# Kernel optimization log

Measured on AMD Instinct MI355X. Metric: run time of the kernel, lower is better.

## Reference

```python
import jax, jax.numpy as jnp
import numpy as np

N = 20000      # nodes
E = 320000     # edges (before self loops)
IN = 128       # in_channels
HID = 256      # hidden_channels
HEADS = 8
C = HID // HEADS  # 32 per-head dim
L = 4          # num_gat_layers
BN_EPS = 1e-5
LN_EPS = 1e-5


def setup_inputs() -> dict:
    key = jax.random.key(0)
    ks = iter(jax.random.split(key, 64))
    def rn(shape, s=0.05):
        return jax.random.normal(next(ks), shape, jnp.float32) * s
    inp = {
        'x': jax.random.normal(next(ks), (N, IN), jnp.float32),
        'edge_index': jax.random.randint(next(ks), (2, E), 0, N),
        # FeatureMLP
        'mlp_w1': rn((IN, HID)), 'mlp_b1': jnp.zeros((HID,), jnp.float32),
        'bn1_g': jnp.ones((HID,), jnp.float32), 'bn1_b': jnp.zeros((HID,), jnp.float32),
        'mlp_w2': rn((HID, HID)), 'mlp_b2': jnp.zeros((HID,), jnp.float32),
        'bn2_g': jnp.ones((HID,), jnp.float32), 'bn2_b': jnp.zeros((HID,), jnp.float32),
        'mlp_w3': rn((HID, HID)), 'mlp_b3': jnp.zeros((HID,), jnp.float32),
        # stacked GATv2 layer params [L, ...]
        'gat_wl': rn((L, HID, HID)), 'gat_bl': jnp.zeros((L, HID), jnp.float32),
        'gat_wr': rn((L, HID, HID)), 'gat_br': jnp.zeros((L, HID), jnp.float32),
        'gat_att': rn((L, HEADS, C)), 'gat_bias': jnp.zeros((L, HID), jnp.float32),
        'ln_g': jnp.ones((L, HID), jnp.float32), 'ln_b': jnp.zeros((L, HID), jnp.float32),
        'head_w1': rn((2 * HID, HID)), 'head_b1': jnp.zeros((HID,), jnp.float32),
        'hbn1_g': jnp.ones((HID,), jnp.float32), 'hbn1_b': jnp.zeros((HID,), jnp.float32),
        'head_w2': rn((HID, HID // 2)), 'head_b2': jnp.zeros((HID // 2,), jnp.float32),
        'hbn2_g': jnp.ones((HID // 2,), jnp.float32), 'hbn2_b': jnp.zeros((HID // 2,), jnp.float32),
        'head_w3': rn((HID // 2, HID // 4)), 'head_b3': jnp.zeros((HID // 4,), jnp.float32),
        'head_w4': rn((HID // 4, 1)), 'head_b4': jnp.zeros((1,), jnp.float32),
    }
    return inp


def _lrelu01(v):
    return jax.nn.leaky_relu(v, 0.1)


def _bn_eval(v, g, b):
    # eval-mode BatchNorm1d with running_mean=0, running_var=1
    return v * (g / jnp.sqrt(1.0 + BN_EPS)) + b


def _layernorm(v, g, b):
    mu = jnp.mean(v, axis=-1, keepdims=True)
    var = jnp.mean((v - mu) ** 2, axis=-1, keepdims=True)
    return (v - mu) / jnp.sqrt(var + LN_EPS) * g + b


def _gatv2(x, src, dst, Wl, bl, Wr, br, att, bias):
    n = x.shape[0]
    xl = (x @ Wl + bl).reshape(n, HEADS, C)   # source transform
    xr = (x @ Wr + br).reshape(n, HEADS, C)   # target transform
    # per-edge attention logits (GATv2): a . LeakyReLU(x_l[src] + x_r[dst])
    e = jax.nn.leaky_relu(xl[src] + xr[dst], 0.2)          # [E, H, C]
    logits = jnp.einsum('ehc,hc->eh', e, att)               # [E, H]
    # segment softmax over destination nodes
    m = jax.ops.segment_max(logits, dst, num_segments=n)    # [N, H]
    a = jnp.exp(logits - m[dst])
    s = jax.ops.segment_sum(a, dst, num_segments=n)
    alpha = a / (s[dst] + 1e-16)                            # [E, H]
    out = jax.ops.segment_sum(xl[src] * alpha[:, :, None], dst, num_segments=n)
    return out.reshape(n, HID) + bias


def _forward(x, mlp_w1, mlp_b1, bn1_g, bn1_b, mlp_w2, mlp_b2, bn2_g, bn2_b,
             mlp_w3, mlp_b3, gat_wl, gat_bl, gat_wr, gat_br, gat_att, gat_bias,
             ln_g, ln_b, head_w1, head_b1, hbn1_g, hbn1_b, head_w2, head_b2,
             hbn2_g, hbn2_b, head_w3, head_b3, head_w4, head_b4, edge_index):
    n = x.shape[0]
    # FeatureMLP (eval: dropout off)
    h = _lrelu01(_bn_eval(x @ mlp_w1 + mlp_b1, bn1_g, bn1_b))
    h = _lrelu01(_bn_eval(h @ mlp_w2 + mlp_b2, bn2_g, bn2_b))
    x_mlp = h @ mlp_w3 + mlp_b3
    # add self loops
    loop = jnp.arange(n)
    src = jnp.concatenate([edge_index[0], loop])
    dst = jnp.concatenate([edge_index[1], loop])
    g = x_mlp
    for i in range(L):
        res = g
        o = _gatv2(g, src, dst, gat_wl[i], gat_bl[i], gat_wr[i], gat_br[i],
                   gat_att[i], gat_bias[i])
        o = _lrelu01(_layernorm(o, ln_g[i], ln_b[i]))
        g = o + res
    xc = jnp.concatenate([x_mlp, g], axis=1)                # [N, 2*HID]
    h = _lrelu01(_bn_eval(xc @ head_w1 + head_b1, hbn1_g, hbn1_b))
    h = _lrelu01(_bn_eval(h @ head_w2 + head_b2, hbn2_g, hbn2_b))
    h = _lrelu01(h @ head_w3 + head_b3)
    return h @ head_w4 + head_b4                            # [N, 1]


def reference(x, edge_index, mlp_w1, mlp_b1, bn1_g, bn1_b, mlp_w2, mlp_b2,
              bn2_g, bn2_b, mlp_w3, mlp_b3, gat_wl, gat_bl, gat_wr, gat_br,
              gat_att, gat_bias, ln_g, ln_b, head_w1, head_b1, hbn1_g, hbn1_b,
              head_w2, head_b2, hbn2_g, hbn2_b, head_w3, head_b3, head_w4, head_b4):
    return _forward(x, mlp_w1, mlp_b1, bn1_g, bn1_b, mlp_w2, mlp_b2, bn2_g,
                    bn2_b, mlp_w3, mlp_b3, gat_wl, gat_bl, gat_wr, gat_br,
                    gat_att, gat_bias, ln_g, ln_b, head_w1, head_b1, hbn1_g,
                    hbn1_b, head_w2, head_b2, hbn2_g, hbn2_b, head_w3, head_b3,
                    head_w4, head_b4, edge_index)
```

## Files before the change

kernel.cpp:

```cpp
#include <hip/hip_runtime.h>
#include <hip/hip_bf16.h>

#define N_NODES 20000
#define E_EDGES 320000
#define E_TOT   (E_EDGES + N_NODES)
#define IN_CH   128
#define HID     256
#define HEADS   8
#define CPH     32

enum { EP_BIAS = 0, EP_BN_LRELU = 1, EP_LRELU = 2 };

typedef _Float16 f16;
typedef f16  f16x2 __attribute__((ext_vector_type(2)));
typedef f16  f16x4 __attribute__((ext_vector_type(4)));
typedef f16  f16x8 __attribute__((ext_vector_type(8)));
typedef float f32x2 __attribute__((ext_vector_type(2)));
typedef float f32x4 __attribute__((ext_vector_type(4)));

__device__ __forceinline__ f16x2 h2max(f16x2 a, f16x2 b) {
#if __has_builtin(__builtin_elementwise_max)
    return __builtin_elementwise_max(a, b);
#else
    f16x2 r; r[0] = a[0] > b[0] ? a[0] : b[0]; r[1] = a[1] > b[1] ? a[1] : b[1]; return r;
#endif
}
__device__ __forceinline__ float hdot2(f16x2 a, f16x2 b, float c) {
#if __has_builtin(__builtin_amdgcn_fdot2)
    return __builtin_amdgcn_fdot2(a, b, c, false);
#else
    return c + (float)a[0] * (float)b[0] + (float)a[1] * (float)b[1];
#endif
}
__device__ __forceinline__ float fexp2(float x) {
#if __has_builtin(__builtin_amdgcn_exp2f)
    return __builtin_amdgcn_exp2f(x);
#else
    return exp2f(x);
#endif
}

__device__ __forceinline__ size_t frag_idx(int row, int col, int KB) {
    int kb = col >> 6, ks = (col >> 5) & 1, q = (col >> 3) & 3, e = col & 7;
    return ((((size_t)(row >> 4) * KB + kb) * 2 + ks) << 9) + (((q << 4) | (row & 15)) << 3) + e;
}

struct WDesc { const float* src; f16* dst; int K; int Nc; int NTOT; int ct0; };
struct WDescs { WDesc d[14]; };

#define WPREP_BLKS (14 * 512)
#define CVT_BLKS   ((N_NODES * IN_CH) / 256)
#define DEG_BLKS   ((E_EDGES + 255) / 256)
#define ZERO_BLKS  ((N_NODES + 255) / 256)
#define PREP_BLKS  (WPREP_BLKS + CVT_BLKS + DEG_BLKS + ZERO_BLKS)

__global__ __launch_bounds__(256)
void prep_kernel(WDescs ds, const float* __restrict__ x, f16* __restrict__ x16,
                 const int* __restrict__ dstE, int* __restrict__ cnt, int* __restrict__ cur)
{
    const int bx = blockIdx.x;
    const int tid = threadIdx.x;
    if (bx < WPREP_BLKS) {
        WDesc w = ds.d[bx >> 9];
        int i = ((bx & 511) << 8) + tid;
        if (i < w.K * w.Nc) {
            int NT_local = w.Nc >> 4;
            int e  = i & 7;
            int l  = (i >> 3) & 63;
            int r  = i >> 9;
            int ct = r % NT_local;
            int q  = r / NT_local;
            int ks = q & 1;
            int kb = q >> 1;
            int n  = ct * 16 + (l & 15);
            int k  = kb * 64 + ks * 32 + ((l >> 4) << 3) + e;
            size_t di = (((size_t)(kb * 2 + ks) * w.NTOT + w.ct0 + ct) << 9) + (l << 3) + e;
            w.dst[di] = (f16)w.src[(size_t)k * w.Nc + n];
        }
    } else if (bx < WPREP_BLKS + CVT_BLKS) {
        int i = (bx - WPREP_BLKS) * 256 + tid;
        if (i < N_NODES * IN_CH) {
            int row = i / IN_CH, col = i - row * IN_CH;
            x16[frag_idx(row, col, 2)] = (f16)x[i];
        }
    } else if (bx < WPREP_BLKS + CVT_BLKS + DEG_BLKS) {
        int e = (bx - WPREP_BLKS - CVT_BLKS) * 256 + tid;
        if (e < E_EDGES) atomicAdd(&cnt[dstE[e]], 1);
    } else {
        int i = (bx - WPREP_BLKS - CVT_BLKS - DEG_BLKS) * 256 + tid;
        if (i < N_NODES) cur[i] = 0;
    }
}

template<int NT, int NTOT, int WAVES, int RT, int DOT, int OUTF>
__global__ __launch_bounds__(WAVES * 64)
void gemm_kernel(const f16* __restrict__ A1, int KB1,
                 const f16* __restrict__ A2, int KB2,
                 const f16* __restrict__ Wf,
                 const float* __restrict__ biasA,
                 const float* __restrict__ biasB,
                 const float* __restrict__ bng,
                 const float* __restrict__ bnb,
                 f16* __restrict__ out16A,
                 f16* __restrict__ out16B,
                 f16* __restrict__ dup16,
                 float* __restrict__ out32,
                 const float* __restrict__ dotw,
                 const float* __restrict__ dotb,
                 float* __restrict__ outdot,
                 int NcA, int KBo, int mode)
{
    __shared__ float red[DOT ? 16 : 1][DOT ? 65 : 1];
    const int tid  = threadIdx.x;
    const int wave = tid >> 6;
    const int lane = tid & 63;
    const int quad = lane >> 4;
    const int rb0 = blockIdx.x * RT;
    const int KBt = KB1 + KB2;

    f32x4 acc[RT][NT];
#pragma unroll
    for (int t = 0; t < RT; ++t)
#pragma unroll
        for (int j = 0; j < NT; ++j) acc[t][j] = (f32x4){0.f, 0.f, 0.f, 0.f};

#pragma unroll 2
    for (int kb = 0; kb < KBt; ++kb) {
#pragma unroll
        for (int ks = 0; ks < 2; ++ks) {
            f16x8 a[RT];
#pragma unroll
            for (int t = 0; t < RT; ++t) {
                const f16* ap = (kb < KB1)
                    ? A1 + (((((size_t)(rb0 + t)) * KB1 + kb) * 2 + ks) << 9) + (lane << 3)
                    : A2 + (((((size_t)(rb0 + t)) * KB2 + (kb - KB1)) * 2 + ks) << 9) + (lane << 3);
                a[t] = *(const f16x8*)ap;
            }
            const f16* bp = Wf + (((size_t)(kb * 2 + ks) * NTOT + wave * NT) << 9) + (lane << 3);
#pragma unroll
            for (int ct = 0; ct < NT; ++ct) {
                f16x8 b = *(const f16x8*)(bp + ((size_t)ct << 9));
#pragma unroll
                for (int t = 0; t < RT; ++t)
                    acc[t][ct] = __builtin_amdgcn_mfma_f32_16x16x32_f16(a[t], b, acc[t][ct], 0, 0, 0);
            }
        }
    }

    const int c0 = lane & 15;
    const int NcB = NTOT * 16 - NcA;
#pragma unroll
    for (int t = 0; t < RT; ++t) {
        const int r0 = (rb0 + t) * 16 + (quad << 2);
#pragma unroll
        for (int ct = 0; ct < NT; ++ct) {
            int col = (wave * NT + ct) * 16 + c0;
            bool isB = col >= NcA;
            int colL = isB ? col - NcA : col;
            float bv = isB ? biasB[colL] : biasA[colL];
            float sc = 1.f, sh = 0.f;
            if (mode == EP_BN_LRELU) {
                sc = bng[col] * rsqrtf(1.f + 1e-5f);
                sh = bnb[col];
            }
#pragma unroll
            for (int reg = 0; reg < 4; ++reg) {
                int row = r0 + reg;
                float v = acc[t][ct][reg] + bv;
                if (mode == EP_BN_LRELU) { v = v * sc + sh; v = v > 0.f ? v : 0.1f * v; }
                else if (mode == EP_LRELU) { v = v > 0.f ? v : 0.1f * v; }
                if (DOT) {
                    red[(quad << 2) + reg][col] = v * dotw[col];
                } else if (row < N_NODES) {
                    if (OUTF) {
                        size_t idx = frag_idx(row, col, KBo);
                        out16A[idx] = (f16)v;
                        if (dup16) dup16[idx] = (f16)v;
                        if (out32) out32[(size_t)row * NcA + col] = v;
                    } else {
                        f16* Cout = isB ? out16B : out16A;
                        int stride = isB ? NcB : NcA;
                        Cout[(size_t)row * stride + colL] = (f16)v;
                    }
                }
            }
        }
    }

    if (DOT) {
        __syncthreads();
        if (wave == 0) {
            int r = lane & 15, q = lane >> 4;
            float psum = 0.f;
#pragma unroll
            for (int j = 0; j < 16; ++j) psum += red[r][q * 16 + j];
            psum += __shfl_xor(psum, 16, 64);
            psum += __shfl_xor(psum, 32, 64);
            if (lane < 16) outdot[rb0 * 16 + r] = psum + dotb[0];
        }
    }
}

__global__ __launch_bounds__(1024)
void scan_kernel(const int* __restrict__ cnt, int* __restrict__ off) {
    __shared__ int wsum[16];
    const int tid = threadIdx.x, wv = tid >> 6, ln = tid & 63;
    const int base = tid * 20;
    int pre[20];
    int loc = 0;
#pragma unroll
    for (int j = 0; j < 20; ++j) {
        int i = base + j;
        int c = (i < N_NODES) ? cnt[i] + 1 : 0;
        pre[j] = loc;
        loc += c;
    }
    int s = loc;
#pragma unroll
    for (int d = 1; d < 64; d <<= 1) { int t = __shfl_up(s, d, 64); if (ln >= d) s += t; }
    if (ln == 63) wsum[wv] = s;
    __syncthreads();
    int woff = 0;
#pragma unroll
    for (int j = 0; j < 16; ++j) if (j < wv) woff += wsum[j];
    int excl = woff + s - loc;
#pragma unroll
    for (int j = 0; j < 20; ++j) {
        int i = base + j;
        if (i < N_NODES) off[i] = excl + pre[j];
    }
    if (tid == 1023) off[N_NODES] = woff + s;
}

__global__ void fill_kernel(const int* __restrict__ src, const int* __restrict__ dst,
                            const int* __restrict__ off, int* __restrict__ cur, int* __restrict__ csr) {
    int i = blockIdx.x * 256 + threadIdx.x;
    if (i < E_EDGES) {
        int d = dst[i];
        int pos = atomicAdd(&cur[d], 1);
        csr[off[d] + pos] = src[i];
    } else {
        int j = i - E_EDGES;
        if (j < N_NODES) csr[off[j + 1] - 1] = j;
    }
}

__global__ __launch_bounds__(256)
void gat_agg_kernel(const f16* __restrict__ xl, const f16* __restrict__ xr,
                    float* __restrict__ g, f16* __restrict__ g16,
                    const int* __restrict__ off, const int* __restrict__ csr,
                    const float* __restrict__ att,
                    const float* __restrict__ bias,
                    const float* __restrict__ lng,
                    const float* __restrict__ lnb)
{
    const int wv   = threadIdx.x >> 6;
    const int ln   = threadIdx.x & 63;
    const int half = ln >> 5;
    const int lp   = ln & 31;
    const int n    = blockIdx.x * 4 + wv;
    if (n >= N_NODES) return;

    const f16x8* xl8 = (const f16x8*)xl;
    f16x8 xrv = ((const f16x8*)xr)[n * 32 + lp];
    f16x2 xr0; xr0[0] = xrv[0]; xr0[1] = xrv[1];
    f16x2 xr1; xr1[0] = xrv[2]; xr1[1] = xrv[3];
    f16x2 xr2; xr2[0] = xrv[4]; xr2[1] = xrv[5];
    f16x2 xr3; xr3[0] = xrv[6]; xr3[1] = xrv[7];
    float4 af0 = ((const float4*)att)[lp * 2];
    float4 af1 = ((const float4*)att)[lp * 2 + 1];
    const float L2E = 1.44269504f;
    f16x2 av0; av0[0] = (f16)(af0.x * L2E); av0[1] = (f16)(af0.y * L2E);
    f16x2 av1; av1[0] = (f16)(af0.z * L2E); av1[1] = (f16)(af0.w * L2E);
    f16x2 av2; av2[0] = (f16)(af1.x * L2E); av2[1] = (f16)(af1.y * L2E);
    f16x2 av3; av3[0] = (f16)(af1.z * L2E); av3[1] = (f16)(af1.w * L2E);
    const f16x2 k02 = { (f16)0.2f, (f16)0.2f };

    float s = 0.f;
    float o0 = 0.f, o1 = 0.f, o2 = 0.f, o3 = 0.f, o4 = 0.f, o5 = 0.f, o6 = 0.f, o7 = 0.f;

    int p = off[n], end = off[n + 1];

    auto procv = [&](f16x8 xv, bool valid) {
        f16x2 x0; x0[0] = xv[0]; x0[1] = xv[1];
        f16x2 x1; x1[0] = xv[2]; x1[1] = xv[3];
        f16x2 x2; x2[0] = xv[4]; x2[1] = xv[5];
        f16x2 x3; x3[0] = xv[6]; x3[1] = xv[7];
        f16x2 v0 = x0 + xr0, v1 = x1 + xr1, v2 = x2 + xr2, v3 = x3 + xr3;
        v0 = h2max(v0, v0 * k02); v1 = h2max(v1, v1 * k02);
        v2 = h2max(v2, v2 * k02); v3 = h2max(v3, v3 * k02);
        float pr = hdot2(v0, av0, hdot2(v1, av1, hdot2(v2, av2, hdot2(v3, av3, 0.f))));
        pr += __shfl_xor(pr, 1, 64);
        pr += __shfl_xor(pr, 2, 64);
        float e = valid ? fexp2(pr) : 0.f;
        s += e;
        o0 = fmaf((float)xv[0], e, o0); o1 = fmaf((float)xv[1], e, o1);
        o2 = fmaf((float)xv[2], e, o2); o3 = fmaf((float)xv[3], e, o3);
        o4 = fmaf((float)xv[4], e, o4); o5 = fmaf((float)xv[5], e, o5);
        o6 = fmaf((float)xv[6], e, o6); o7 = fmaf((float)xv[7], e, o7);
    };
    auto proc = [&](int ep) {
        bool valid = ep < end;
        int sidx = csr[valid ? ep : end - 1];
        procv(xl8[(size_t)sidx * 32 + lp], valid);
    };

    for (; p + 8 <= end; p += 8) {
        int sA = csr[p +     half];
        int sB = csr[p + 2 + half];
        int sC = csr[p + 4 + half];
        int sD = csr[p + 6 + half];
        f16x8 rA = xl8[(size_t)sA * 32 + lp];
        f16x8 rB = xl8[(size_t)sB * 32 + lp];
        f16x8 rC = xl8[(size_t)sC * 32 + lp];
        f16x8 rD = xl8[(size_t)sD * 32 + lp];
        procv(rA, true); procv(rB, true); procv(rC, true); procv(rD, true);
    }
    for (; p + 4 <= end; p += 4) {
        int sA = csr[p +     half];
        int sB = csr[p + 2 + half];
        f16x8 rA = xl8[(size_t)sA * 32 + lp];
        f16x8 rB = xl8[(size_t)sB * 32 + lp];
        procv(rA, true); procv(rB, true);
    }
    for (; p < end; p += 2) proc(p + half);

    s  += __shfl_xor(s, 32, 64);
    o0 += __shfl_xor(o0, 32, 64); o1 += __shfl_xor(o1, 32, 64);
    o2 += __shfl_xor(o2, 32, 64); o3 += __shfl_xor(o3, 32, 64);
    o4 += __shfl_xor(o4, 32, 64); o5 += __shfl_xor(o5, 32, 64);
    o6 += __shfl_xor(o6, 32, 64); o7 += __shfl_xor(o7, 32, 64);

    const int lidx = lp * 2 + half;
    float q0 = half ? o4 : o0;
    float q1 = half ? o5 : o1;
    float q2 = half ? o6 : o2;
    float q3 = half ? o7 : o3;

    float inv = 1.f / (s + 1e-16f);
    float4 bi = ((const float4*)bias)[lidx];
    float y0 = q0 * inv + bi.x;
    float y1 = q1 * inv + bi.y;
    float y2 = q2 * inv + bi.z;
    float y3 = q3 * inv + bi.w;

    float s1 = y0 + y1 + y2 + y3;
    float s2 = y0 * y0 + y1 * y1 + y2 * y2 + y3 * y3;
#pragma unroll
    for (int d = 32; d; d >>= 1) { s1 += __shfl_xor(s1, d, 64); s2 += __shfl_xor(s2, d, 64); }
    float mu  = s1 * (1.f / HID);
    float ex2 = s2 * (1.f / HID);
    float rstd = rsqrtf(ex2 - mu * mu + 1e-5f);
    float4 lg = ((const float4*)lng)[lidx];
    float4 lb = ((const float4*)lnb)[lidx];
    float nv0 = (y0 - mu) * rstd * lg.x + lb.x; nv0 = nv0 > 0.f ? nv0 : 0.1f * nv0;
    float nv1 = (y1 - mu) * rstd * lg.y + lb.y; nv1 = nv1 > 0.f ? nv1 : 0.1f * nv1;
    float nv2 = (y2 - mu) * rstd * lg.z + lb.z; nv2 = nv2 > 0.f ? nv2 : 0.1f * nv2;
    float nv3 = (y3 - mu) * rstd * lg.w + lb.w; nv3 = nv3 > 0.f ? nv3 : 0.1f * nv3;

    float4 gv = ((const float4*)g)[n * 64 + lidx];
    float g0 = nv0 + gv.x, g1 = nv1 + gv.y, g2 = nv2 + gv.z, g3 = nv3 + gv.w;
    ((float4*)g)[n * 64 + lidx] = make_float4(g0, g1, g2, g3);
    f16x4 gh; gh[0] = (f16)g0; gh[1] = (f16)g1; gh[2] = (f16)g2; gh[3] = (f16)g3;
    *(f16x4*)&g16[frag_idx(n, 4 * lidx, 4)] = gh;
}

static inline size_t align_up(size_t v, size_t a) { return (v + a - 1) & ~(a - 1); }

extern "C" void kernel_launch(void* const* d_in, const int* in_sizes, int n_in,
                              void* d_out, int out_size, void* d_ws, size_t ws_size,
                              hipStream_t stream)
{
    const float* x      = (const float*)d_in[0];
    const int*   ei     = (const int*)d_in[1];
    const float* mlp_w1 = (const float*)d_in[2];
    const float* mlp_b1 = (const float*)d_in[3];
    const float* bn1_g  = (const float*)d_in[4];
    const float* bn1_b  = (const float*)d_in[5];
    const float* mlp_w2 = (const float*)d_in[6];
    const float* mlp_b2 = (const float*)d_in[7];
    const float* bn2_g  = (const float*)d_in[8];
    const float* bn2_b  = (const float*)d_in[9];
    const float* mlp_w3 = (const float*)d_in[10];
    const float* mlp_b3 = (const float*)d_in[11];
    const float* gat_wl = (const float*)d_in[12];
    const float* gat_bl = (const float*)d_in[13];
    const float* gat_wr = (const float*)d_in[14];
    const float* gat_br = (const float*)d_in[15];
    const float* gat_att  = (const float*)d_in[16];
    const float* gat_bias = (const float*)d_in[17];
    const float* ln_g   = (const float*)d_in[18];
    const float* ln_b   = (const float*)d_in[19];
    const float* head_w1 = (const float*)d_in[20];
    const float* head_b1 = (const float*)d_in[21];
    const float* hbn1_g  = (const float*)d_in[22];
    const float* hbn1_b  = (const float*)d_in[23];
    const float* head_w2 = (const float*)d_in[24];
    const float* head_b2 = (const float*)d_in[25];
    const float* hbn2_g  = (const float*)d_in[26];
    const float* hbn2_b  = (const float*)d_in[27];
    const float* head_w3 = (const float*)d_in[28];
    const float* head_b3 = (const float*)d_in[29];
    const float* head_w4 = (const float*)d_in[30];
    const float* head_b4 = (const float*)d_in[31];
    float* out = (float*)d_out;

    char* w = (char*)d_ws;
    size_t p = 0;
    int* off  = (int*)(w + p); p = align_up(p + (N_NODES + 1) * sizeof(int), 64);
    int* fill = (int*)(w + p); p = align_up(p + N_NODES * sizeof(int), 64);
    int* cur  = (int*)(w + p); p = align_up(p + N_NODES * sizeof(int), 64);
    int* csr  = (int*)(w + p); p = align_up(p + E_TOT * sizeof(int), 64);
    float* g32 = (float*)(w + p); p = align_up(p + (size_t)N_NODES * HID * 4, 64);
    auto halloc = [&](size_t elems) {
        f16* q = (f16*)(w + p);
        p = align_up(p + elems * 2, 1024);
        return q;
    };
    f16* x16     = halloc((size_t)N_NODES * IN_CH);
    f16* h1      = halloc((size_t)N_NODES * HID);
    f16* h2      = halloc((size_t)N_NODES * HID);
    f16* x_mlp16 = halloc((size_t)N_NODES * HID);
    f16* g16     = halloc((size_t)N_NODES * HID);
    f16* xl16    = halloc((size_t)N_NODES * HID);
    f16* xr16    = halloc((size_t)N_NODES * HID);
    f16* wt_mlp1 = halloc((size_t)IN_CH * HID);
    f16* wt_mlp2 = halloc((size_t)HID * HID);
    f16* wt_mlp3 = halloc((size_t)HID * HID);
    f16* wt_g[4];
    for (int i = 0; i < 4; ++i) wt_g[i] = halloc((size_t)HID * 2 * HID);
    f16* wt_h1 = halloc((size_t)2 * HID * HID);
    f16* wt_h2 = halloc((size_t)HID * (HID / 2));
    f16* wt_h3 = halloc((size_t)(HID / 2) * (HID / 4));
    (void)ws_size; (void)in_sizes; (void)n_in; (void)out_size;

    const int* e_src = ei;
    const int* e_dst = ei + E_EDGES;

    dim3 blk(256);
    dim3 gM313((N_NODES + 63) / 64);
    dim3 gM1250((N_NODES + 15) / 16);

    WDescs ds;
    ds.d[0]  = { mlp_w1, wt_mlp1, IN_CH, HID, 16, 0 };
    ds.d[1]  = { mlp_w2, wt_mlp2, HID, HID, 16, 0 };
    ds.d[2]  = { mlp_w3, wt_mlp3, HID, HID, 16, 0 };
    for (int i = 0; i < 4; ++i) {
        ds.d[3 + 2 * i] = { gat_wl + (size_t)i * HID * HID, wt_g[i], HID, HID, 32, 0 };
        ds.d[4 + 2 * i] = { gat_wr + (size_t)i * HID * HID, wt_g[i], HID, HID, 32, 16 };
    }
    ds.d[11] = { head_w1, wt_h1, 2 * HID, HID, 16, 0 };
    ds.d[12] = { head_w2, wt_h2, HID, HID / 2, 8, 0 };
    ds.d[13] = { head_w3, wt_h3, HID / 2, HID / 4, 4, 0 };

    hipMemsetAsync(fill, 0, N_NODES * sizeof(int), stream);
    prep_kernel<<<dim3(PREP_BLKS), blk, 0, stream>>>(ds, x, x16, e_dst, fill, cur);
    scan_kernel<<<1, 1024, 0, stream>>>(fill, off);
    fill_kernel<<<(E_TOT + 255) / 256, blk, 0, stream>>>(e_src, e_dst, off, cur, csr);

    gemm_kernel<2, 16, 8, 4, 0, 1><<<gM313, 512, 0, stream>>>(x16, 2, nullptr, 0, wt_mlp1, mlp_b1, mlp_b1,
        bn1_g, bn1_b, h1, nullptr, nullptr, nullptr, nullptr, nullptr, nullptr, HID, 4, EP_BN_LRELU);
    gemm_kernel<2, 16, 8, 4, 0, 1><<<gM313, 512, 0, stream>>>(h1, 4, nullptr, 0, wt_mlp2, mlp_b2, mlp_b2,
        bn2_g, bn2_b, h2, nullptr, nullptr, nullptr, nullptr, nullptr, nullptr, HID, 4, EP_BN_LRELU);
    gemm_kernel<2, 16, 8, 4, 0, 1><<<gM313, 512, 0, stream>>>(h2, 4, nullptr, 0, wt_mlp3, mlp_b3, mlp_b3,
        nullptr, nullptr, x_mlp16, nullptr, g16, g32, nullptr, nullptr, nullptr, HID, 4, EP_BIAS);

    for (int i = 0; i < 4; ++i) {
        gemm_kernel<4, 32, 8, 4, 0, 0><<<gM313, 512, 0, stream>>>(g16, 4, nullptr, 0, wt_g[i],
            gat_bl + i * HID, gat_br + i * HID, nullptr, nullptr,
            xl16, xr16, nullptr, nullptr, nullptr, nullptr, nullptr, HID, 0, EP_BIAS);
        gat_agg_kernel<<<(N_NODES + 3) / 4, blk, 0, stream>>>(xl16, xr16, g32, g16, off, csr,
                                                              gat_att + i * HID, gat_bias + i * HID,
                                                              ln_g + i * HID, ln_b + i * HID);
    }

    gemm_kernel<2, 16, 8, 4, 0, 1><<<gM313, 512, 0, stream>>>(x_mlp16, 4, g16, 4, wt_h1, head_b1, head_b1,
        hbn1_g, hbn1_b, h1, nullptr, nullptr, nullptr, nullptr, nullptr, nullptr, HID, 4, EP_BN_LRELU);
    gemm_kernel<1, 8, 8, 4, 0, 1><<<gM313, 512, 0, stream>>>(h1, 4, nullptr, 0, wt_h2, head_b2, head_b2,
        hbn2_g, hbn2_b, h2, nullptr, nullptr, nullptr, nullptr, nullptr, nullptr, HID / 2, 2, EP_BN_LRELU);
    gemm_kernel<1, 4, 4, 1, 1, 0><<<gM1250, 256, 0, stream>>>(h2, 2, nullptr, 0, wt_h3, head_b3, head_b3,
        nullptr, nullptr, nullptr, nullptr, nullptr, nullptr, head_w4, head_b4, out, HID / 4, 0, EP_LRELU);
}
```

Before: 466.7 us.

## Fuse GAT layers into one persistent kernel with grid barriers

Replaces the eight per-layer GEMM and aggregation launches with a single persistent kernel of 256 blocks. The blocks loop over all four layers, alternating the linear projection and the attention aggregation, separated by atomic-counter grid barriers. Other GEMMs switch to 32-row tiles (RT=2) with twice as many blocks, and the row bounds check is dropped because N divides evenly. This trades launch overhead and idle tails between kernels for barrier spin cost and lower occupancy. It also risks deadlock if not all 256 blocks are co-resident.

```diff
diff --git a/kernel.cpp b/kernel.cpp
--- a/kernel.cpp
+++ b/kernel.cpp
@@ -56,7 +56,8 @@
 
 __global__ __launch_bounds__(256)
 void prep_kernel(WDescs ds, const float* __restrict__ x, f16* __restrict__ x16,
-                 const int* __restrict__ dstE, int* __restrict__ cnt, int* __restrict__ cur)
+                 const int* __restrict__ dstE, int* __restrict__ cnt, int* __restrict__ cur,
+                 int* __restrict__ bar)
 {
     const int bx = blockIdx.x;
     const int tid = threadIdx.x;
@@ -89,6 +90,7 @@
     } else {
         int i = (bx - WPREP_BLKS - CVT_BLKS - DEG_BLKS) * 256 + tid;
         if (i < N_NODES) cur[i] = 0;
+        if (bx == WPREP_BLKS + CVT_BLKS + DEG_BLKS && tid < 16) bar[tid] = 0;
     }
 }
 
@@ -171,7 +173,7 @@
                 else if (mode == EP_LRELU) { v = v > 0.f ? v : 0.1f * v; }
                 if (DOT) {
                     red[(quad << 2) + reg][col] = v * dotw[col];
-                } else if (row < N_NODES) {
+                } else {
                     if (OUTF) {
                         size_t idx = frag_idx(row, col, KBo);
                         out16A[idx] = (f16)v;
@@ -245,124 +247,205 @@
     }
 }
 
-__global__ __launch_bounds__(256)
-void gat_agg_kernel(const f16* __restrict__ xl, const f16* __restrict__ xr,
-                    float* __restrict__ g, f16* __restrict__ g16,
-                    const int* __restrict__ off, const int* __restrict__ csr,
-                    const float* __restrict__ att,
-                    const float* __restrict__ bias,
-                    const float* __restrict__ lng,
-                    const float* __restrict__ lnb)
+#define PERSIST_GRID 256
+
+__device__ __forceinline__ void gbar(int* bar, int target) {
+    __threadfence();
+    __syncthreads();
+    if (threadIdx.x == 0) {
+        __hip_atomic_fetch_add(bar, 1, __ATOMIC_RELEASE, __HIP_MEMORY_SCOPE_AGENT);
+        while (__hip_atomic_load(bar, __ATOMIC_ACQUIRE, __HIP_MEMORY_SCOPE_AGENT) < target)
+            __builtin_amdgcn_s_sleep(4);
+    }
+    __syncthreads();
+    __threadfence();
+}
+
+struct GatFusedArgs {
+    f16* xl; f16* xr; float* g32; f16* g16;
+    const int* off; const int* csr;
+    const float* att; const float* bias; const float* lng; const float* lnb;
+    const float* bl; const float* br;
+    const f16* wt0; const f16* wt1; const f16* wt2; const f16* wt3;
+    int* bar;
+};
+
+__global__ __launch_bounds__(512)
+void gat_persist_kernel(GatFusedArgs A)
 {
-    const int wv   = threadIdx.x >> 6;
-    const int ln   = threadIdx.x & 63;
-    const int half = ln >> 5;
-    const int lp   = ln & 31;
-    const int n    = blockIdx.x * 4 + wv;
-    if (n >= N_NODES) return;
-
-    const f16x8* xl8 = (const f16x8*)xl;
-    f16x8 xrv = ((const f16x8*)xr)[n * 32 + lp];
-    f16x2 xr0; xr0[0] = xrv[0]; xr0[1] = xrv[1];
-    f16x2 xr1; xr1[0] = xrv[2]; xr1[1] = xrv[3];
-    f16x2 xr2; xr2[0] = xrv[4]; xr2[1] = xrv[5];
-    f16x2 xr3; xr3[0] = xrv[6]; xr3[1] = xrv[7];
-    float4 af0 = ((const float4*)att)[lp * 2];
-    float4 af1 = ((const float4*)att)[lp * 2 + 1];
+    const int tid  = threadIdx.x;
+    const int wave = tid >> 6;
+    const int lane = tid & 63;
+    const int quad = lane >> 4;
+    const int c0   = lane & 15;
+    const int bid  = blockIdx.x;
+    const int half = lane >> 5;
+    const int lp   = lane & 31;
+    const int lidx = lp * 2 + half;
+    const f16x8* xl8 = (const f16x8*)A.xl;
+    const f16x2 k02 = { (f16)0.2f, (f16)0.2f };
     const float L2E = 1.44269504f;
-    f16x2 av0; av0[0] = (f16)(af0.x * L2E); av0[1] = (f16)(af0.y * L2E);
-    f16x2 av1; av1[0] = (f16)(af0.z * L2E); av1[1] = (f16)(af0.w * L2E);
-    f16x2 av2; av2[0] = (f16)(af1.x * L2E); av2[1] = (f16)(af1.y * L2E);
-    f16x2 av3; av3[0] = (f16)(af1.z * L2E); av3[1] = (f16)(af1.w * L2E);
-    const f16x2 k02 = { (f16)0.2f, (f16)0.2f };
-
-    float s = 0.f;
-    float o0 = 0.f, o1 = 0.f, o2 = 0.f, o3 = 0.f, o4 = 0.f, o5 = 0.f, o6 = 0.f, o7 = 0.f;
-
-    int p = off[n], end = off[n + 1];
-
-    auto procv = [&](f16x8 xv, bool valid) {
-        f16x2 x0; x0[0] = xv[0]; x0[1] = xv[1];
-        f16x2 x1; x1[0] = xv[2]; x1[1] = xv[3];
-        f16x2 x2; x2[0] = xv[4]; x2[1] = xv[5];
-        f16x2 x3; x3[0] = xv[6]; x3[1] = xv[7];
-        f16x2 v0 = x0 + xr0, v1 = x1 + xr1, v2 = x2 + xr2, v3 = x3 + xr3;
-        v0 = h2max(v0, v0 * k02); v1 = h2max(v1, v1 * k02);
-        v2 = h2max(v2, v2 * k02); v3 = h2max(v3, v3 * k02);
-        float pr = hdot2(v0, av0, hdot2(v1, av1, hdot2(v2, av2, hdot2(v3, av3, 0.f))));
-        pr += __shfl_xor(pr, 1, 64);
-        pr += __shfl_xor(pr, 2, 64);
-        float e = valid ? fexp2(pr) : 0.f;
-        s += e;
-        o0 = fmaf((float)xv[0], e, o0); o1 = fmaf((float)xv[1], e, o1);
-        o2 = fmaf((float)xv[2], e, o2); o3 = fmaf((float)xv[3], e, o3);
-        o4 = fmaf((float)xv[4], e, o4); o5 = fmaf((float)xv[5], e, o5);
-        o6 = fmaf((float)xv[6], e, o6); o7 = fmaf((float)xv[7], e, o7);
-    };
-    auto proc = [&](int ep) {
-        bool valid = ep < end;
-        int sidx = csr[valid ? ep : end - 1];
-        procv(xl8[(size_t)sidx * 32 + lp], valid);
-    };
-
-    for (; p + 8 <= end; p += 8) {
-        int sA = csr[p +     half];
-        int sB = csr[p + 2 + half];
-        int sC = csr[p + 4 + half];
-        int sD = csr[p + 6 + half];
-        f16x8 rA = xl8[(size_t)sA * 32 + lp];
-        f16x8 rB = xl8[(size_t)sB * 32 + lp];
-        f16x8 rC = xl8[(size_t)sC * 32 + lp];
-        f16x8 rD = xl8[(size_t)sD * 32 + lp];
-        procv(rA, true); procv(rB, true); procv(rC, true); procv(rD, true);
-    }
-    for (; p + 4 <= end; p += 4) {
-        int sA = csr[p +     half];
-        int sB = csr[p + 2 + half];
-        f16x8 rA = xl8[(size_t)sA * 32 + lp];
-        f16x8 rB = xl8[(size_t)sB * 32 + lp];
-        procv(rA, true); procv(rB, true);
-    }
-    for (; p < end; p += 2) proc(p + half);
-
-    s  += __shfl_xor(s, 32, 64);
-    o0 += __shfl_xor(o0, 32, 64); o1 += __shfl_xor(o1, 32, 64);
-    o2 += __shfl_xor(o2, 32, 64); o3 += __shfl_xor(o3, 32, 64);
-    o4 += __shfl_xor(o4, 32, 64); o5 += __shfl_xor(o5, 32, 64);
-    o6 += __shfl_xor(o6, 32, 64); o7 += __shfl_xor(o7, 32, 64);
-
-    const int lidx = lp * 2 + half;
-    float q0 = half ? o4 : o0;
-    float q1 = half ? o5 : o1;
-    float q2 = half ? o6 : o2;
-    float q3 = half ? o7 : o3;
-
-    float inv = 1.f / (s + 1e-16f);
-    float4 bi = ((const float4*)bias)[lidx];
-    float y0 = q0 * inv + bi.x;
-    float y1 = q1 * inv + bi.y;
-    float y2 = q2 * inv + bi.z;
-    float y3 = q3 * inv + bi.w;
-
-    float s1 = y0 + y1 + y2 + y3;
-    float s2 = y0 * y0 + y1 * y1 + y2 * y2 + y3 * y3;
-#pragma unroll
-    for (int d = 32; d; d >>= 1) { s1 += __shfl_xor(s1, d, 64); s2 += __shfl_xor(s2, d, 64); }
-    float mu  = s1 * (1.f / HID);
-    float ex2 = s2 * (1.f / HID);
-    float rstd = rsqrtf(ex2 - mu * mu + 1e-5f);
-    float4 lg = ((const float4*)lng)[lidx];
-    float4 lb = ((const float4*)lnb)[lidx];
-    float nv0 = (y0 - mu) * rstd * lg.x + lb.x; nv0 = nv0 > 0.f ? nv0 : 0.1f * nv0;
-    float nv1 = (y1 - mu) * rstd * lg.y + lb.y; nv1 = nv1 > 0.f ? nv1 : 0.1f * nv1;
-    float nv2 = (y2 - mu) * rstd * lg.z + lb.z; nv2 = nv2 > 0.f ? nv2 : 0.1f * nv2;
-    float nv3 = (y3 - mu) * rstd * lg.w + lb.w; nv3 = nv3 > 0.f ? nv3 : 0.1f * nv3;
-
-    float4 gv = ((const float4*)g)[n * 64 + lidx];
-    float g0 = nv0 + gv.x, g1 = nv1 + gv.y, g2 = nv2 + gv.z, g3 = nv3 + gv.w;
-    ((float4*)g)[n * 64 + lidx] = make_float4(g0, g1, g2, g3);
-    f16x4 gh; gh[0] = (f16)g0; gh[1] = (f16)g1; gh[2] = (f16)g2; gh[3] = (f16)g3;
-    *(f16x4*)&g16[frag_idx(n, 4 * lidx, 4)] = gh;
+    int tgt = 0;
+
+    for (int layer = 0; layer < 4; ++layer) {
+        const f16* Wf = layer == 0 ? A.wt0 : layer == 1 ? A.wt1 : layer == 2 ? A.wt2 : A.wt3;
+        const float* biasL = A.bl + layer * HID;
+        const float* biasR = A.br + layer * HID;
+        for (int pr = bid; pr < 625; pr += PERSIST_GRID) {
+            const int rb0 = pr * 2;
+            f32x4 acc[2][4];
+#pragma unroll
+            for (int t = 0; t < 2; ++t)
+#pragma unroll
+                for (int j = 0; j < 4; ++j) acc[t][j] = (f32x4){0.f, 0.f, 0.f, 0.f};
+#pragma unroll 2
+            for (int kb = 0; kb < 4; ++kb) {
+#pragma unroll
+                for (int ks = 0; ks < 2; ++ks) {
+                    f16x8 a[2];
+#pragma unroll
+                    for (int t = 0; t < 2; ++t)
+                        a[t] = *(const f16x8*)(A.g16 + (((((size_t)(rb0 + t)) * 4 + kb) * 2 + ks) << 9) + (lane << 3));
+                    const f16* bp = Wf + (((size_t)(kb * 2 + ks) * 32 + wave * 4) << 9) + (lane << 3);
+#pragma unroll
+                    for (int ct = 0; ct < 4; ++ct) {
+                        f16x8 b = *(const f16x8*)(bp + ((size_t)ct << 9));
+#pragma unroll
+                        for (int t = 0; t < 2; ++t)
+                            acc[t][ct] = __builtin_amdgcn_mfma_f32_16x16x32_f16(a[t], b, acc[t][ct], 0, 0, 0);
+                    }
+                }
+            }
+#pragma unroll
+            for (int t = 0; t < 2; ++t) {
+                const int r0 = (rb0 + t) * 16 + (quad << 2);
+#pragma unroll
+                for (int ct = 0; ct < 4; ++ct) {
+                    int col = (wave * 4 + ct) * 16 + c0;
+                    bool isR = col >= HID;
+                    int colL = col & (HID - 1);
+                    float bv = isR ? biasR[colL] : biasL[colL];
+                    f16* Cout = isR ? A.xr : A.xl;
+#pragma unroll
+                    for (int reg = 0; reg < 4; ++reg)
+                        Cout[(size_t)(r0 + reg) * HID + colL] = (f16)(acc[t][ct][reg] + bv);
+                }
+            }
+        }
+        tgt += PERSIST_GRID;
+        gbar(A.bar, tgt);
+
+        {
+            const float* att   = A.att  + layer * HID;
+            const float* biasv = A.bias + layer * HID;
+            const float* lng   = A.lng  + layer * HID;
+            const float* lnb   = A.lnb  + layer * HID;
+            float4 af0 = ((const float4*)att)[lp * 2];
+            float4 af1 = ((const float4*)att)[lp * 2 + 1];
+            f16x2 av0; av0[0] = (f16)(af0.x * L2E); av0[1] = (f16)(af0.y * L2E);
+            f16x2 av1; av1[0] = (f16)(af0.z * L2E); av1[1] = (f16)(af0.w * L2E);
+            f16x2 av2; av2[0] = (f16)(af1.x * L2E); av2[1] = (f16)(af1.y * L2E);
+            f16x2 av3; av3[0] = (f16)(af1.z * L2E); av3[1] = (f16)(af1.w * L2E);
+            float4 bi = ((const float4*)biasv)[lidx];
+            float4 lg = ((const float4*)lng)[lidx];
+            float4 lb = ((const float4*)lnb)[lidx];
+
+            for (int n = bid * 8 + wave; n < N_NODES; n += PERSIST_GRID * 8) {
+                f16x8 xrv = ((const f16x8*)A.xr)[n * 32 + lp];
+                f16x2 xr0; xr0[0] = xrv[0]; xr0[1] = xrv[1];
+                f16x2 xr1; xr1[0] = xrv[2]; xr1[1] = xrv[3];
+                f16x2 xr2; xr2[0] = xrv[4]; xr2[1] = xrv[5];
+                f16x2 xr3; xr3[0] = xrv[6]; xr3[1] = xrv[7];
+
+                float s = 0.f;
+                float o0 = 0.f, o1 = 0.f, o2 = 0.f, o3 = 0.f, o4 = 0.f, o5 = 0.f, o6 = 0.f, o7 = 0.f;
+                int p = A.off[n], end = A.off[n + 1];
+
+                auto procv = [&](f16x8 xv, bool valid) {
+                    f16x2 x0; x0[0] = xv[0]; x0[1] = xv[1];
+                    f16x2 x1; x1[0] = xv[2]; x1[1] = xv[3];
+                    f16x2 x2; x2[0] = xv[4]; x2[1] = xv[5];
+                    f16x2 x3; x3[0] = xv[6]; x3[1] = xv[7];
+                    f16x2 v0 = x0 + xr0, v1 = x1 + xr1, v2 = x2 + xr2, v3 = x3 + xr3;
+                    v0 = h2max(v0, v0 * k02); v1 = h2max(v1, v1 * k02);
+                    v2 = h2max(v2, v2 * k02); v3 = h2max(v3, v3 * k02);
+                    float pr = hdot2(v0, av0, hdot2(v1, av1, hdot2(v2, av2, hdot2(v3, av3, 0.f))));
+                    pr += __shfl_xor(pr, 1, 64);
+                    pr += __shfl_xor(pr, 2, 64);
+                    float e = valid ? fexp2(pr) : 0.f;
+                    s += e;
+                    o0 = fmaf((float)xv[0], e, o0); o1 = fmaf((float)xv[1], e, o1);
+                    o2 = fmaf((float)xv[2], e, o2); o3 = fmaf((float)xv[3], e, o3);
+                    o4 = fmaf((float)xv[4], e, o4); o5 = fmaf((float)xv[5], e, o5);
+                    o6 = fmaf((float)xv[6], e, o6); o7 = fmaf((float)xv[7], e, o7);
+                };
+
+                for (; p + 8 <= end; p += 8) {
+                    int sA = A.csr[p +     half];
+                    int sB = A.csr[p + 2 + half];
+                    int sC = A.csr[p + 4 + half];
+                    int sD = A.csr[p + 6 + half];
+                    f16x8 rA = xl8[(size_t)sA * 32 + lp];
+                    f16x8 rB = xl8[(size_t)sB * 32 + lp];
+                    f16x8 rC = xl8[(size_t)sC * 32 + lp];
+                    f16x8 rD = xl8[(size_t)sD * 32 + lp];
+                    procv(rA, true); procv(rB, true); procv(rC, true); procv(rD, true);
+                }
+                for (; p + 4 <= end; p += 4) {
+                    int sA = A.csr[p +     half];
+                    int sB = A.csr[p + 2 + half];
+                    f16x8 rA = xl8[(size_t)sA * 32 + lp];
+                    f16x8 rB = xl8[(size_t)sB * 32 + lp];
+                    procv(rA, true); procv(rB, true);
+                }
+                for (; p < end; p += 2) {
+                    int ep = p + half;
+                    bool valid = ep < end;
+                    int sidx = A.csr[valid ? ep : end - 1];
+                    procv(xl8[(size_t)sidx * 32 + lp], valid);
+                }
+
+                s  += __shfl_xor(s, 32, 64);
+                o0 += __shfl_xor(o0, 32, 64); o1 += __shfl_xor(o1, 32, 64);
+                o2 += __shfl_xor(o2, 32, 64); o3 += __shfl_xor(o3, 32, 64);
+                o4 += __shfl_xor(o4, 32, 64); o5 += __shfl_xor(o5, 32, 64);
+                o6 += __shfl_xor(o6, 32, 64); o7 += __shfl_xor(o7, 32, 64);
+
+                float q0 = half ? o4 : o0;
+                float q1 = half ? o5 : o1;
+                float q2 = half ? o6 : o2;
+                float q3 = half ? o7 : o3;
+
+                float inv = 1.f / (s + 1e-16f);
+                float y0 = q0 * inv + bi.x;
+                float y1 = q1 * inv + bi.y;
+                float y2 = q2 * inv + bi.z;
+                float y3 = q3 * inv + bi.w;
+
+                float s1 = y0 + y1 + y2 + y3;
+                float s2 = y0 * y0 + y1 * y1 + y2 * y2 + y3 * y3;
+#pragma unroll
+                for (int d = 32; d; d >>= 1) { s1 += __shfl_xor(s1, d, 64); s2 += __shfl_xor(s2, d, 64); }
+                float mu  = s1 * (1.f / HID);
+                float ex2 = s2 * (1.f / HID);
+                float rstd = rsqrtf(ex2 - mu * mu + 1e-5f);
+                float nv0 = (y0 - mu) * rstd * lg.x + lb.x; nv0 = nv0 > 0.f ? nv0 : 0.1f * nv0;
+                float nv1 = (y1 - mu) * rstd * lg.y + lb.y; nv1 = nv1 > 0.f ? nv1 : 0.1f * nv1;
+                float nv2 = (y2 - mu) * rstd * lg.z + lb.z; nv2 = nv2 > 0.f ? nv2 : 0.1f * nv2;
+                float nv3 = (y3 - mu) * rstd * lg.w + lb.w; nv3 = nv3 > 0.f ? nv3 : 0.1f * nv3;
+
+                float4 gv = ((const float4*)A.g32)[n * 64 + lidx];
+                float g0 = nv0 + gv.x, g1 = nv1 + gv.y, g2 = nv2 + gv.z, g3 = nv3 + gv.w;
+                ((float4*)A.g32)[n * 64 + lidx] = make_float4(g0, g1, g2, g3);
+                f16x4 gh; gh[0] = (f16)g0; gh[1] = (f16)g1; gh[2] = (f16)g2; gh[3] = (f16)g3;
+                *(f16x4*)&A.g16[frag_idx(n, 4 * lidx, 4)] = gh;
+            }
+        }
+        if (layer < 3) {
+            tgt += PERSIST_GRID;
+            gbar(A.bar, tgt);
+        }
+    }
 }
 
 static inline size_t align_up(size_t v, size_t a) { return (v + a - 1) & ~(a - 1); }
@@ -410,6 +493,7 @@
     int* off  = (int*)(w + p); p = align_up(p + (N_NODES + 1) * sizeof(int), 64);
     int* fill = (int*)(w + p); p = align_up(p + N_NODES * sizeof(int), 64);
     int* cur  = (int*)(w + p); p = align_up(p + N_NODES * sizeof(int), 64);
+    int* bar  = (int*)(w + p); p = align_up(p + 16 * sizeof(int), 64);
     int* csr  = (int*)(w + p); p = align_up(p + E_TOT * sizeof(int), 64);
     float* g32 = (float*)(w + p); p = align_up(p + (size_t)N_NODES * HID * 4, 64);
     auto halloc = [&](size_t elems) {
@@ -438,7 +522,7 @@
     const int* e_dst = ei + E_EDGES;
 
     dim3 blk(256);
-    dim3 gM313((N_NODES + 63) / 64);
+    dim3 gM625((N_NODES + 31) / 32);
     dim3 gM1250((N_NODES + 15) / 16);
 
     WDescs ds;
@@ -454,29 +538,29 @@
     ds.d[13] = { head_w3, wt_h3, HID / 2, HID / 4, 4, 0 };
 
     hipMemsetAsync(fill, 0, N_NODES * sizeof(int), stream);
-    prep_kernel<<<dim3(PREP_BLKS), blk, 0, stream>>>(ds, x, x16, e_dst, fill, cur);
+    prep_kernel<<<dim3(PREP_BLKS), blk, 0, stream>>>(ds, x, x16, e_dst, fill, cur, bar);
     scan_kernel<<<1, 1024, 0, stream>>>(fill, off);
     fill_kernel<<<(E_TOT + 255) / 256, blk, 0, stream>>>(e_src, e_dst, off, cur, csr);
 
-    gemm_kernel<2, 16, 8, 4, 0, 1><<<gM313, 512, 0, stream>>>(x16, 2, nullptr, 0, wt_mlp1, mlp_b1, mlp_b1,
+    gemm_kernel<2, 16, 8, 2, 0, 1><<<gM625, 512, 0, stream>>>(x16, 2, nullptr, 0, wt_mlp1, mlp_b1, mlp_b1,
         bn1_g, bn1_b, h1, nullptr, nullptr, nullptr, nullptr, nullptr, nullptr, HID, 4, EP_BN_LRELU);
-    gemm_kernel<2, 16, 8, 4, 0, 1><<<gM313, 512, 0, stream>>>(h1, 4, nullptr, 0, wt_mlp2, mlp_b2, mlp_b2,
+    gemm_kernel<2, 16, 8, 2, 0, 1><<<gM625, 512, 0, stream>>>(h1, 4, nullptr, 0, wt_mlp2, mlp_b2, mlp_b2,
         bn2_g, bn2_b, h2, nullptr, nullptr, nullptr, nullptr, nullptr, nullptr, HID, 4, EP_BN_LRELU);
-    gemm_kernel<2, 16, 8, 4, 0, 1><<<gM313, 512, 0, stream>>>(h2, 4, nullptr, 0, wt_mlp3, mlp_b3, mlp_b3,
+    gemm_kernel<2, 16, 8, 2, 0, 1><<<gM625, 512, 0, stream>>>(h2, 4, nullptr, 0, wt_mlp3, mlp_b3, mlp_b3,
         nullptr, nullptr, x_mlp16, nullptr, g16, g32, nullptr, nullptr, nullptr, HID, 4, EP_BIAS);
 
-    for (int i = 0; i < 4; ++i) {
-        gemm_kernel<4, 32, 8, 4, 0, 0><<<gM313, 512, 0, stream>>>(g16, 4, nullptr, 0, wt_g[i],
-            gat_bl + i * HID, gat_br + i * HID, nullptr, nullptr,
-            xl16, xr16, nullptr, nullptr, nullptr, nullptr, nullptr, HID, 0, EP_BIAS);
-        gat_agg_kernel<<<(N_NODES + 3) / 4, blk, 0, stream>>>(xl16, xr16, g32, g16, off, csr,
-                                                              gat_att + i * HID, gat_bias + i * HID,
-                                                              ln_g + i * HID, ln_b + i * HID);
-    }
-
-    gemm_kernel<2, 16, 8, 4, 0, 1><<<gM313, 512, 0, stream>>>(x_mlp16, 4, g16, 4, wt_h1, head_b1, head_b1,
+    GatFusedArgs fa;
+    fa.xl = xl16; fa.xr = xr16; fa.g32 = g32; fa.g16 = g16;
+    fa.off = off; fa.csr = csr;
+    fa.att = gat_att; fa.bias = gat_bias; fa.lng = ln_g; fa.lnb = ln_b;
+    fa.bl = gat_bl; fa.br = gat_br;
+    fa.wt0 = wt_g[0]; fa.wt1 = wt_g[1]; fa.wt2 = wt_g[2]; fa.wt3 = wt_g[3];
+    fa.bar = bar;
+    gat_persist_kernel<<<dim3(PERSIST_GRID), dim3(512), 0, stream>>>(fa);
+
+    gemm_kernel<2, 16, 8, 2, 0, 1><<<gM625, 512, 0, stream>>>(x_mlp16, 4, g16, 4, wt_h1, head_b1, head_b1,
         hbn1_g, hbn1_b, h1, nullptr, nullptr, nullptr, nullptr, nullptr, nullptr, HID, 4, EP_BN_LRELU);
-    gemm_kernel<1, 8, 8, 4, 0, 1><<<gM313, 512, 0, stream>>>(h1, 4, nullptr, 0, wt_h2, head_b2, head_b2,
+    gemm_kernel<1, 8, 8, 2, 0, 1><<<gM625, 512, 0, stream>>>(h1, 4, nullptr, 0, wt_h2, head_b2, head_b2,
         hbn2_g, hbn2_b, h2, nullptr, nullptr, nullptr, nullptr, nullptr, nullptr, HID / 2, 2, EP_BN_LRELU);
     gemm_kernel<1, 4, 4, 1, 1, 0><<<gM1250, 256, 0, stream>>>(h2, 2, nullptr, 0, wt_h3, head_b3, head_b3,
         nullptr, nullptr, nullptr, nullptr, nullptr, nullptr, head_w4, head_b4, out, HID / 4, 0, EP_LRELU);
```

Result: slower. 1.491 ms (+219.5%).
